# Optimization experiments

Hardware: AMD Instinct MI355X
Metric: run time of the kernel (lower is better)

The kernel has to match this reference:

```python
import jax, jax.numpy as jnp
import numpy as np

B, N_IN, N_OUT, D_IN, D_OUT = 64, 1152, 10, 8, 16

def setup_inputs() -> dict:
    key = jax.random.key(0)
    k1, k2 = jax.random.split(key)
    # inputs: [B, num_in_caps, in_caps_dims[0]=8, in_caps_dims[1]=1]
    inputs = jax.random.normal(k1, (B, N_IN, D_IN, 1), dtype=jnp.float32)
    # transform matrix: prefix_shape + [in0, out0, 1] = [1, N_IN, N_OUT, 8, 16, 1]
    # TF random_uniform_initializer default: U(-0.05, 0.05)
    transform_mat = jax.random.uniform(
        k2, (1, N_IN, N_OUT, D_IN, D_OUT, 1), dtype=jnp.float32,
        minval=-0.05, maxval=0.05)
    return {"inputs": inputs, "transform_mat": transform_mat}

def reference(inputs, transform_mat):
    # Branch: in_caps_dims[1] == out_caps_dims[1] (== 1).
    # Original TF math (broadcast-multiply + reduce_sum over axis -3):
    #   in_pose[b,n,m,i,1,1] * W[1,n,m,i,o,1] summed over i
    # => votes[b,n,m,o,0] = sum_i inputs[b,n,i,0] * W[0,n,m,i,o,0]
    votes = jnp.einsum('bni,nmio->bnmo', inputs[..., 0], transform_mat[0, ..., 0])
    return votes[..., None]  # [B, N_IN, N_OUT, D_OUT, 1]
```

## Files before the change

kernel.cpp:

```cpp
#include <hip/hip_runtime.h>


typedef float floatx4 __attribute__((ext_vector_type(4)));

constexpr int B     = 64;
constexpr int N_IN  = 1152;
constexpr int N_OUT = 10;
constexpr int D_IN  = 8;
constexpr int D_OUT = 16;
constexpr int KB    = 16;
constexpr int NBB   = B / KB;
constexpr int NCHUNK = N_IN * N_OUT * 4 / 256;
constexpr int NBLOCKS = NCHUNK * NBB;
constexpr int MAIN  = 176 * NBB;

__global__ __launch_bounds__(256)
void Transforming_56195352101061_kernel(const float* __restrict__ in,
                                        const float* __restrict__ W,
                                        float* __restrict__ out) {
    int id = blockIdx.x;
    int bb, c;
    if (id < MAIN) {
        int r = id & 7;
        int t = id >> 3;
        bb    = t & 3;
        c     = (t >> 2) * 8 + r;
    } else {
        int k = id - MAIN;
        bb    = k >> 2;
        c     = 176 + (k & 3);
    }

    int tid = c * 256 + (int)threadIdx.x;
    int o4  = tid & 3;
    int lin = tid >> 2;
    int m   = lin % N_OUT;
    int n   = lin / N_OUT;

    const float* wbase = W + ((size_t)(n * N_OUT + m) * D_IN) * D_OUT + o4 * 4;
    floatx4 w[D_IN];
#pragma unroll
    for (int i = 0; i < D_IN; ++i)
        w[i] = *reinterpret_cast<const floatx4*>(wbase + i * D_OUT);

    const float* ibase = in + ((size_t)(bb * KB) * N_IN + n) * D_IN;
    floatx4* out4 = reinterpret_cast<floatx4*>(out);
    size_t obase = ((size_t)((bb * KB) * N_IN + n) * N_OUT + m) * 4 + o4;
    constexpr size_t OB_STRIDE = (size_t)N_IN * N_OUT * 4;

#pragma unroll 4
    for (int j = 0; j < KB; ++j) {
        const floatx4* iv = reinterpret_cast<const floatx4*>(
            ibase + (size_t)j * N_IN * D_IN);
        floatx4 i0 = iv[0];
        floatx4 i1 = iv[1];
        float ivals[8] = {i0.x, i0.y, i0.z, i0.w, i1.x, i1.y, i1.z, i1.w};

        floatx4 acc = {0.f, 0.f, 0.f, 0.f};
#pragma unroll
        for (int i = 0; i < D_IN; ++i)
            acc += ivals[i] * w[i];

        __builtin_nontemporal_store(acc, &out4[obase + (size_t)j * OB_STRIDE]);
    }
}

extern "C" void kernel_launch(void* const* d_in, const int* in_sizes, int n_in,
                              void* d_out, int out_size, void* d_ws, size_t ws_size,
                              hipStream_t stream) {
    const float* in = (const float*)d_in[0];
    const float* W  = (const float*)d_in[1];
    float* out      = (float*)d_out;

    Transforming_56195352101061_kernel<<<NBLOCKS, 256, 0, stream>>>(in, W, out);
}
```

Measured before the change: 14.22 us.

## Process all batches per thread with 64-thread blocks, dropping batch split

Each thread now loops over all 64 batch entries instead of 16, so each weight float4 set is loaded once rather than four times. Blocks shrink to 64 threads and the custom block-index remapping over batch groups is removed. This cuts redundant weight loads, but the grid drops to a quarter as many waves, which reduces the memory parallelism available to hide latency in this store-heavy kernel.

```diff
diff --git a/kernel.cpp b/kernel.cpp
--- a/kernel.cpp
+++ b/kernel.cpp
@@ -8,30 +8,15 @@
 constexpr int N_OUT = 10;
 constexpr int D_IN  = 8;
 constexpr int D_OUT = 16;
-constexpr int KB    = 16;
-constexpr int NBB   = B / KB;
-constexpr int NCHUNK = N_IN * N_OUT * 4 / 256;
-constexpr int NBLOCKS = NCHUNK * NBB;
-constexpr int MAIN  = 176 * NBB;
+constexpr int NT4   = N_IN * N_OUT * 4;
+constexpr int BLOCK = 64;
+constexpr int NBLOCKS = NT4 / BLOCK;
 
-__global__ __launch_bounds__(256)
+__global__ __launch_bounds__(BLOCK)
 void Transforming_56195352101061_kernel(const float* __restrict__ in,
                                         const float* __restrict__ W,
                                         float* __restrict__ out) {
-    int id = blockIdx.x;
-    int bb, c;
-    if (id < MAIN) {
-        int r = id & 7;
-        int t = id >> 3;
-        bb    = t & 3;
-        c     = (t >> 2) * 8 + r;
-    } else {
-        int k = id - MAIN;
-        bb    = k >> 2;
-        c     = 176 + (k & 3);
-    }
-
-    int tid = c * 256 + (int)threadIdx.x;
+    int tid = blockIdx.x * BLOCK + (int)threadIdx.x;
     int o4  = tid & 3;
     int lin = tid >> 2;
     int m   = lin % N_OUT;
@@ -43,15 +28,13 @@
     for (int i = 0; i < D_IN; ++i)
         w[i] = *reinterpret_cast<const floatx4*>(wbase + i * D_OUT);
 
-    const float* ibase = in + ((size_t)(bb * KB) * N_IN + n) * D_IN;
-    floatx4* out4 = reinterpret_cast<floatx4*>(out);
-    size_t obase = ((size_t)((bb * KB) * N_IN + n) * N_OUT + m) * 4 + o4;
-    constexpr size_t OB_STRIDE = (size_t)N_IN * N_OUT * 4;
+    const float* ibase = in + (size_t)n * D_IN;
+    floatx4* out4 = reinterpret_cast<floatx4*>(out) + tid;
 
-#pragma unroll 4
-    for (int j = 0; j < KB; ++j) {
+#pragma unroll 8
+    for (int b = 0; b < B; ++b) {
         const floatx4* iv = reinterpret_cast<const floatx4*>(
-            ibase + (size_t)j * N_IN * D_IN);
+            ibase + (size_t)b * N_IN * D_IN);
         floatx4 i0 = iv[0];
         floatx4 i1 = iv[1];
         float ivals[8] = {i0.x, i0.y, i0.z, i0.w, i1.x, i1.y, i1.z, i1.w};
@@ -61,7 +44,7 @@
         for (int i = 0; i < D_IN; ++i)
             acc += ivals[i] * w[i];
 
-        __builtin_nontemporal_store(acc, &out4[obase + (size_t)j * OB_STRIDE]);
+        __builtin_nontemporal_store(acc, out4 + (size_t)b * NT4);
     }
 }
 
@@ -72,5 +55,5 @@
     const float* W  = (const float*)d_in[1];
     float* out      = (float*)d_out;
 
-    Transforming_56195352101061_kernel<<<NBLOCKS, 256, 0, stream>>>(in, W, out);
+    Transforming_56195352101061_kernel<<<NBLOCKS, BLOCK, 0, stream>>>(in, W, out);
 }
```

Result: slower. 17.50 us (+23.1%).
